# Kernel tuning notes

Hardware: AMD Instinct MI355X
Metric: run time of the kernel (lower is better)

Reference implementation:

```python
import jax, jax.numpy as jnp
import numpy as np
import math

NUM_HEADS = 16
LOGIT_SCALE_MAX = math.log(1.0 / 0.01)  # log(100)
EPS = 1e-12


def _l2norm(x):
    # F.normalize(x, dim=-1): x / max(||x||_2, eps)
    n = jnp.sqrt(jnp.sum(x * x, axis=-1, keepdims=True))
    return x / jnp.maximum(n, EPS)


def setup_inputs() -> dict:
    key = jax.random.key(0)
    ks = jax.random.split(key, 6)
    N, B, C = 1024, 4, 1024
    scale = (C // NUM_HEADS) ** -0.5
    return {
        "query": jax.random.normal(ks[0], (N, B, C), jnp.float32),
        "key": jax.random.normal(ks[1], (N, B, C), jnp.float32),
        "value": jax.random.normal(ks[2], (N, B, C), jnp.float32),
        "in_proj_w": jax.random.normal(ks[3], (3 * C, C), jnp.float32) * scale,
        "in_proj_b": jnp.zeros((3 * C,), jnp.float32),
        "logit_scale": jnp.log(10.0) * jnp.ones((NUM_HEADS, 1, 1), jnp.float32),
        "out_w": jax.random.normal(ks[4], (C, C), jnp.float32) * scale,
        "out_b": jnp.zeros((C,), jnp.float32),
    }


def reference(query, key, value, in_proj_w, in_proj_b, logit_scale, out_w, out_b):
    N, B, C = query.shape
    H = NUM_HEADS
    hd = C // H
    # packed in-projection, split into q/k/v pieces
    w_q, w_k, w_v = jnp.split(in_proj_w, 3, axis=0)
    b_q, b_k, b_v = jnp.split(in_proj_b, 3, axis=0)
    q = query @ w_q.T + b_q          # (N, B, C)
    k = key @ w_k.T + b_k
    v = value @ w_v.T + b_v
    # (N, B, C) -> (B*H, N, hd)
    q = q.reshape(N, B * H, hd).swapaxes(0, 1)
    k = k.reshape(N, B * H, hd).swapaxes(0, 1)
    v = v.reshape(N, B * H, hd).swapaxes(0, 1)
    # cosine-similarity scores with learnable per-head logit scale
    attn = jnp.einsum('bqd,bkd->bqk', _l2norm(q), _l2norm(k))  # (B*H, N, N)
    ls = jnp.exp(jnp.minimum(logit_scale, LOGIT_SCALE_MAX))     # (H,1,1)
    attn = (attn.reshape(B, H, N, N) * ls).reshape(B * H, N, N)
    attn = jax.nn.softmax(attn, axis=-1)
    x = jnp.einsum('bqk,bkd->bqd', attn, v)                     # (B*H, N, hd)
    x = x.swapaxes(0, 1).reshape(N, B, C)
    return x @ out_w.T + out_b
```

## Files before the change

### kernel.cpp

```cpp
#include <hip/hip_runtime.h>


typedef _Float16 f16x8 __attribute__((ext_vector_type(8)));
typedef __fp16   fp16x2 __attribute__((ext_vector_type(2)));
typedef float    f32x4 __attribute__((ext_vector_type(4)));

#define LOG2E 1.4426950408889634f
#define LOGMAX 4.6051702f

#define GLOAD16(g, l) \
    __builtin_amdgcn_global_load_lds((__attribute__((address_space(1))) void*)(g), \
                                     (__attribute__((address_space(3))) void*)(l), 16, 0, 0)

__device__ __forceinline__ unsigned short f2h(float x) {
    union { _Float16 h; unsigned short u; } cv;
    cv.h = (_Float16)x;
    return cv.u;
}

union h2u { fp16x2 h; unsigned int u; };

__global__ __launch_bounds__(256) void cvt_all(
    const float* __restrict__ q, const float* __restrict__ k,
    const float* __restrict__ v, const float* __restrict__ w,
    const float* __restrict__ ow,
    unsigned short* __restrict__ qbf, unsigned short* __restrict__ kbf,
    unsigned short* __restrict__ vbf, unsigned short* __restrict__ wbf,
    unsigned short* __restrict__ owbf)
{
    int b = blockIdx.x;
    const float* src; unsigned short* dst; int idx;
    if      (b < 4096)  { src = q;  dst = qbf;  idx = b; }
    else if (b < 8192)  { src = k;  dst = kbf;  idx = b - 4096; }
    else if (b < 12288) { src = v;  dst = vbf;  idx = b - 8192; }
    else if (b < 15360) { src = w;  dst = wbf;  idx = b - 12288; }
    else                { src = ow; dst = owbf; idx = b - 15360; }
    int i = idx * 256 + threadIdx.x;
    float4 val = ((const float4*)src)[i];
    h2u p01, p23;
    p01.h = __builtin_amdgcn_cvt_pkrtz(val.x, val.y);
    p23.h = __builtin_amdgcn_cvt_pkrtz(val.z, val.w);
    ((uint2*)dst)[i] = (uint2){p01.u, p23.u};
}

__global__ __launch_bounds__(256) void proj_gemm(
    const unsigned short* __restrict__ qbf, const unsigned short* __restrict__ kbf,
    const unsigned short* __restrict__ vbf, const unsigned short* __restrict__ wbf,
    const float* __restrict__ bias, const float* __restrict__ lsc,
    unsigned short* __restrict__ qn, unsigned short* __restrict__ kn,
    unsigned short* __restrict__ vT)
{
    __shared__ __align__(16) unsigned short AsmF[128 * 64];
    __shared__ __align__(16) unsigned short BsmF[128 * 64];
    int tid = threadIdx.x;
    int lane = tid & 63, wave = tid >> 6;
    int lr = lane & 15, lq = lane >> 4;
    int wr = wave >> 1, wc = wave & 1;

    int lin = blockIdx.x;
    int xcd = lin & 7, s = lin >> 3;
    int xt = s & 7, yy = (s >> 3) & 3, z = s >> 5;
    int m0 = (xcd * 4 + yy) * 128, n0 = xt * 128;

    const unsigned short* A = (z == 0) ? qbf : (z == 1) ? kbf : vbf;
    const unsigned short* W = wbf + (size_t)z * 1024 * 1024;

    int rl = lane >> 3;
    int cg = ((lane & 7) ^ rl) << 3;
    const unsigned short* gA = A + (size_t)(m0 + wave * 32 + rl) * 1024 + cg;
    const unsigned short* gB = W + (size_t)(n0 + wave * 32 + rl) * 1024 + cg;
    unsigned short* lA = &AsmF[wave * 32 * 64];
    unsigned short* lB = &BsmF[wave * 32 * 64];

    int swz = lr & 7;
    int c0 = (lq ^ swz) << 3;
    int c1 = ((lq ^ 4) ^ swz) << 3;

    f32x4 acc[4][4];
    for (int i = 0; i < 4; i++) for (int j = 0; j < 4; j++) acc[i][j] = (f32x4){0.f, 0.f, 0.f, 0.f};

    for (int ki = 0; ki < 16; ++ki) {
        for (int j = 0; j < 4; ++j) {
            GLOAD16(gA + ki * 64 + j * 8192, lA + j * 512);
            GLOAD16(gB + ki * 64 + j * 8192, lB + j * 512);
        }
        __syncthreads();
        for (int kc = 0; kc < 2; ++kc) {
            int co = kc ? c1 : c0;
            f16x8 af[4], bfr[4];
            for (int mi = 0; mi < 4; ++mi) af[mi]  = *(const f16x8*)&AsmF[(wr * 64 + mi * 16 + lr) * 64 + co];
            for (int ni = 0; ni < 4; ++ni) bfr[ni] = *(const f16x8*)&BsmF[(wc * 64 + ni * 16 + lr) * 64 + co];
            for (int mi = 0; mi < 4; ++mi)
                for (int ni = 0; ni < 4; ++ni)
                    acc[mi][ni] = __builtin_amdgcn_mfma_f32_16x16x32_f16(af[mi], bfr[ni], acc[mi][ni], 0, 0, 0);
        }
        __syncthreads();
    }

    int h = (n0 >> 6) + wc;
    float bv[4];
    for (int ni = 0; ni < 4; ++ni) bv[ni] = bias[z * 1024 + n0 + wc * 64 + ni * 16 + lr];
    for (int mi = 0; mi < 4; ++mi)
        for (int ni = 0; ni < 4; ++ni)
            for (int r = 0; r < 4; ++r) acc[mi][ni][r] += bv[ni];

    float lsfac = __expf(fminf(lsc[h], LOGMAX)) * LOG2E;

    for (int mi = 0; mi < 4; ++mi)
        for (int r = 0; r < 4; ++r) {
            int row = m0 + wr * 64 + mi * 16 + lq * 4 + r;
            int n = row >> 2, b = row & 3;
            int bh = b * 16 + h;
            if (z < 2) {
                float ss = 0.f;
                for (int ni = 0; ni < 4; ++ni) ss += acc[mi][ni][r] * acc[mi][ni][r];
                for (int off = 1; off < 16; off <<= 1) ss += __shfl_xor(ss, off);
                float scale = 1.0f / fmaxf(sqrtf(ss), 1e-12f);
                if (z == 0) scale *= lsfac;
                unsigned short* dst = (z == 0) ? qn : kn;
                for (int ni = 0; ni < 4; ++ni)
                    dst[(size_t)bh * 65536 + (size_t)n * 64 + ni * 16 + lr] = f2h(acc[mi][ni][r] * scale);
            } else {
                for (int ni = 0; ni < 4; ++ni)
                    vT[(size_t)bh * 65536 + (size_t)(ni * 16 + lr) * 1024 + n] = f2h(acc[mi][ni][r]);
            }
        }
}

__global__ __launch_bounds__(256) void flash_kernel(
    const unsigned short* __restrict__ qn, const unsigned short* __restrict__ kn,
    const unsigned short* __restrict__ vT, const float* __restrict__ lsc,
    unsigned short* __restrict__ xb)
{
    __shared__ __align__(16) unsigned short K_flat[64 * 64];
    __shared__ __align__(16) unsigned short V_flat[64 * 64];
    __shared__ __align__(16) unsigned short P_lds[4][2][16][72];
    int tid = threadIdx.x;
    int lane = tid & 63, wave = tid >> 6;
    int lr = lane & 15, lq = lane >> 4;

    int lin = blockIdx.x;
    int xcd = lin & 7, s = lin >> 3;
    int qt = s & 7, bh = xcd * 8 + (s >> 3);
    int q0 = qt * 128;

    float off = __expf(fminf(lsc[bh & 15], LOGMAX)) * LOG2E - 12.0f;
    f32x4 initv = (f32x4){-off, -off, -off, -off};

    f16x8 onev;
    for (int j = 0; j < 8; ++j) onev[j] = (_Float16)1.0f;

    f16x8 qf[2][2];
    for (int g = 0; g < 2; ++g)
        for (int kc = 0; kc < 2; ++kc)
            qf[g][kc] = *(const f16x8*)(qn + (size_t)bh * 65536 +
                          (size_t)(q0 + g * 64 + wave * 16 + lr) * 64 + kc * 32 + lq * 8);

    int rl = lane >> 3;
    int cg = ((lane & 7) ^ rl) << 3;
    const unsigned short* gK = kn + (size_t)bh * 65536 + (size_t)(wave * 16 + rl) * 64 + cg;
    const unsigned short* gV = vT + (size_t)bh * 65536 + (size_t)(wave * 16 + rl) * 1024 + cg;
    unsigned short* lK = &K_flat[wave * 16 * 64];
    unsigned short* lV = &V_flat[wave * 16 * 64];
    int swz = lr & 7;
    int c0 = (lq ^ swz) << 3;
    int c1 = ((lq ^ 4) ^ swz) << 3;

    f32x4 o[2][4];
    for (int g = 0; g < 2; ++g) for (int i = 0; i < 4; i++) o[g][i] = (f32x4){0.f, 0.f, 0.f, 0.f};
    f32x4 ol[2];
    ol[0] = (f32x4){0.f, 0.f, 0.f, 0.f};
    ol[1] = (f32x4){0.f, 0.f, 0.f, 0.f};

    for (int kt = 0; kt < 16; ++kt) {
        for (int j = 0; j < 2; ++j) {
            GLOAD16(gK + kt * 4096 + j * 512,  lK + j * 512);
            GLOAD16(gV + kt * 64  + j * 8192,  lV + j * 512);
        }
        __syncthreads();

        f32x4 sc[2][4];
        for (int ct = 0; ct < 4; ++ct) {
            for (int kc = 0; kc < 2; ++kc) {
                f16x8 kf = *(const f16x8*)&K_flat[(ct * 16 + lr) * 64 + (kc ? c1 : c0)];
                for (int g = 0; g < 2; ++g)
                    sc[g][ct] = __builtin_amdgcn_mfma_f32_16x16x32_f16(
                        kf, qf[g][kc], kc == 0 ? initv : sc[g][ct], 0, 0, 0);
            }
        }

        for (int g = 0; g < 2; ++g)
            for (int ct = 0; ct < 4; ++ct) {
                float p0 = exp2f(sc[g][ct][0]), p1 = exp2f(sc[g][ct][1]);
                float p2 = exp2f(sc[g][ct][2]), p3 = exp2f(sc[g][ct][3]);
                h2u a01, a23;
                a01.h = __builtin_amdgcn_cvt_pkrtz(p0, p1);
                a23.h = __builtin_amdgcn_cvt_pkrtz(p2, p3);
                *(uint2*)&P_lds[wave][g][lr][ct * 16 + lq * 4] = (uint2){a01.u, a23.u};
            }

        f16x8 pf[2][2];
        for (int g = 0; g < 2; ++g)
            for (int kc = 0; kc < 2; ++kc)
                pf[g][kc] = *(const f16x8*)&P_lds[wave][g][lr][kc * 32 + lq * 8];
        for (int g = 0; g < 2; ++g)
            for (int kc = 0; kc < 2; ++kc)
                ol[g] = __builtin_amdgcn_mfma_f32_16x16x32_f16(onev, pf[g][kc], ol[g], 0, 0, 0);
        for (int nt = 0; nt < 4; ++nt)
            for (int kc = 0; kc < 2; ++kc) {
                f16x8 vf = *(const f16x8*)&V_flat[(nt * 16 + lr) * 64 + (kc ? c1 : c0)];
                for (int g = 0; g < 2; ++g)
                    o[g][nt] = __builtin_amdgcn_mfma_f32_16x16x32_f16(vf, pf[g][kc], o[g][nt], 0, 0, 0);
            }
        __syncthreads();
    }

    int b = bh >> 4, h = bh & 15;
    for (int g = 0; g < 2; ++g) {
        float inv = 1.0f / ol[g][0];
        size_t m = (size_t)(q0 + g * 64 + wave * 16 + lr) * 4 + b;
        h2u w01, w23;
        for (int nt = 0; nt < 4; ++nt) {
            w01.h = __builtin_amdgcn_cvt_pkrtz(o[g][nt][0] * inv, o[g][nt][1] * inv);
            w23.h = __builtin_amdgcn_cvt_pkrtz(o[g][nt][2] * inv, o[g][nt][3] * inv);
            *(uint2*)(xb + m * 1024 + h * 64 + nt * 16 + lq * 4) = (uint2){w01.u, w23.u};
        }
    }
}

__global__ __launch_bounds__(256) void out_gemm(
    const unsigned short* __restrict__ xb, const unsigned short* __restrict__ owbf,
    const float* __restrict__ bias, float* __restrict__ outp)
{
    __shared__ __align__(16) unsigned short AsmF[128 * 64];
    __shared__ __align__(16) unsigned short BsmF[64 * 64];
    int tid = threadIdx.x;
    int lane = tid & 63, wave = tid >> 6;
    int lr = lane & 15, lq = lane >> 4;

    int lin = blockIdx.x;
    int xcd = lin & 7, s = lin >> 3;
    int xt = s & 15, yy = s >> 4;
    int m0 = (xcd * 4 + yy) * 128, n0 = xt * 64;

    int rl = lane >> 3;
    int cg = ((lane & 7) ^ rl) << 3;
    const unsigned short* gA = xb   + (size_t)(m0 + wave * 32 + rl) * 1024 + cg;
    const unsigned short* gB = owbf + (size_t)(n0 + wave * 16 + rl) * 1024 + cg;
    unsigned short* lA = &AsmF[wave * 32 * 64];
    unsigned short* lB = &BsmF[wave * 16 * 64];
    int swz = lr & 7;
    int c0 = (lq ^ swz) << 3;
    int c1 = ((lq ^ 4) ^ swz) << 3;

    f32x4 acc[2][4];
    for (int i = 0; i < 2; i++) for (int j = 0; j < 4; j++) acc[i][j] = (f32x4){0.f, 0.f, 0.f, 0.f};

    for (int ki = 0; ki < 16; ++ki) {
        for (int j = 0; j < 4; ++j)
            GLOAD16(gA + ki * 64 + j * 8192, lA + j * 512);
        for (int j = 0; j < 2; ++j)
            GLOAD16(gB + ki * 64 + j * 8192, lB + j * 512);
        __syncthreads();
        for (int kc = 0; kc < 2; ++kc) {
            int co = kc ? c1 : c0;
            f16x8 af[2], bfr[4];
            for (int mi = 0; mi < 2; ++mi) af[mi]  = *(const f16x8*)&AsmF[(wave * 32 + mi * 16 + lr) * 64 + co];
            for (int ni = 0; ni < 4; ++ni) bfr[ni] = *(const f16x8*)&BsmF[(ni * 16 + lr) * 64 + co];
            for (int mi = 0; mi < 2; ++mi)
                for (int ni = 0; ni < 4; ++ni)
                    acc[mi][ni] = __builtin_amdgcn_mfma_f32_16x16x32_f16(af[mi], bfr[ni], acc[mi][ni], 0, 0, 0);
        }
        __syncthreads();
    }
    for (int mi = 0; mi < 2; ++mi)
        for (int ni = 0; ni < 4; ++ni)
            for (int r = 0; r < 4; ++r) {
                int row = m0 + wave * 32 + mi * 16 + lq * 4 + r;
                int col = n0 + ni * 16 + lr;
                outp[(size_t)row * 1024 + col] = acc[mi][ni][r] + bias[col];
            }
}

extern "C" void kernel_launch(void* const* d_in, const int* in_sizes, int n_in,
                              void* d_out, int out_size, void* d_ws, size_t ws_size,
                              hipStream_t stream) {
    const float* query = (const float*)d_in[0];
    const float* key   = (const float*)d_in[1];
    const float* value = (const float*)d_in[2];
    const float* ipw   = (const float*)d_in[3];
    const float* ipb   = (const float*)d_in[4];
    const float* lsc   = (const float*)d_in[5];
    const float* ow    = (const float*)d_in[6];
    const float* ob    = (const float*)d_in[7];
    float* outp = (float*)d_out;

    char* ws = (char*)d_ws;
    unsigned short* qbf  = (unsigned short*)(ws);
    unsigned short* kbf  = (unsigned short*)(ws + 8388608);
    unsigned short* vbf  = (unsigned short*)(ws + 16777216);
    unsigned short* wbf  = (unsigned short*)(ws + 25165824);
    unsigned short* owbf = (unsigned short*)(ws + 31457280);
    unsigned short* qn   = (unsigned short*)(ws + 33554432);
    unsigned short* kn   = (unsigned short*)(ws + 41943040);
    unsigned short* vT   = (unsigned short*)(ws + 50331648);
    unsigned short* xbuf = (unsigned short*)(ws + 58720256);

    cvt_all<<<16384, 256, 0, stream>>>(query, key, value, ipw, ow,
                                       qbf, kbf, vbf, wbf, owbf);
    proj_gemm<<<768, 256, 0, stream>>>(qbf, kbf, vbf, wbf, ipb, lsc, qn, kn, vT);
    flash_kernel<<<512, 256, 0, stream>>>(qn, kn, vT, lsc, xbuf);
    out_gemm<<<512, 256, 0, stream>>>(xbuf, owbf, ob, outp);
}
```

Before: 210.1 us.

## Double-buffer K/V tiles and keep softmax probabilities in registers for PV MFMA

The flash attention kernel now double-buffers the K and V tiles in LDS. The next tile's global-to-LDS loads are issued before computing on the current one, and one of the two barriers per iteration is removed. The P staging round trip through LDS is dropped: the exp'd scores stay in registers as f16x4 fragments that feed 16x16x16 MFMAs directly, with V fragments read in a matching swizzled layout. This trades a doubled LDS footprint and twice as many narrower MFMA instructions for less LDS traffic and better overlap of loads with compute.

```diff
diff --git a/kernel.cpp b/kernel.cpp
--- a/kernel.cpp
+++ b/kernel.cpp
@@ -2,6 +2,7 @@
 
 
 typedef _Float16 f16x8 __attribute__((ext_vector_type(8)));
+typedef _Float16 f16x4 __attribute__((ext_vector_type(4)));
 typedef __fp16   fp16x2 __attribute__((ext_vector_type(2)));
 typedef float    f32x4 __attribute__((ext_vector_type(4)));
 
@@ -19,6 +20,7 @@
 }
 
 union h2u { fp16x2 h; unsigned int u; };
+union u2h4 { uint2 u; f16x4 h; };
 
 __global__ __launch_bounds__(256) void cvt_all(
     const float* __restrict__ q, const float* __restrict__ k,
@@ -132,9 +134,8 @@
     const unsigned short* __restrict__ vT, const float* __restrict__ lsc,
     unsigned short* __restrict__ xb)
 {
-    __shared__ __align__(16) unsigned short K_flat[64 * 64];
-    __shared__ __align__(16) unsigned short V_flat[64 * 64];
-    __shared__ __align__(16) unsigned short P_lds[4][2][16][72];
+    __shared__ __align__(16) unsigned short K_flat[2][64 * 64];
+    __shared__ __align__(16) unsigned short V_flat[2][64 * 64];
     int tid = threadIdx.x;
     int lane = tid & 63, wave = tid >> 6;
     int lr = lane & 15, lq = lane >> 4;
@@ -147,8 +148,8 @@
     float off = __expf(fminf(lsc[bh & 15], LOGMAX)) * LOG2E - 12.0f;
     f32x4 initv = (f32x4){-off, -off, -off, -off};
 
-    f16x8 onev;
-    for (int j = 0; j < 8; ++j) onev[j] = (_Float16)1.0f;
+    f16x4 onev4;
+    for (int j = 0; j < 4; ++j) onev4[j] = (_Float16)1.0f;
 
     f16x8 qf[2][2];
     for (int g = 0; g < 2; ++g)
@@ -160,8 +161,6 @@
     int cg = ((lane & 7) ^ rl) << 3;
     const unsigned short* gK = kn + (size_t)bh * 65536 + (size_t)(wave * 16 + rl) * 64 + cg;
     const unsigned short* gV = vT + (size_t)bh * 65536 + (size_t)(wave * 16 + rl) * 1024 + cg;
-    unsigned short* lK = &K_flat[wave * 16 * 64];
-    unsigned short* lV = &V_flat[wave * 16 * 64];
     int swz = lr & 7;
     int c0 = (lq ^ swz) << 3;
     int c1 = ((lq ^ 4) ^ swz) << 3;
@@ -172,23 +171,35 @@
     ol[0] = (f32x4){0.f, 0.f, 0.f, 0.f};
     ol[1] = (f32x4){0.f, 0.f, 0.f, 0.f};
 
+    for (int j = 0; j < 2; ++j) {
+        GLOAD16(gK + j * 512,  &K_flat[0][wave * 16 * 64] + j * 512);
+        GLOAD16(gV + j * 8192, &V_flat[0][wave * 16 * 64] + j * 512);
+    }
+
     for (int kt = 0; kt < 16; ++kt) {
-        for (int j = 0; j < 2; ++j) {
-            GLOAD16(gK + kt * 4096 + j * 512,  lK + j * 512);
-            GLOAD16(gV + kt * 64  + j * 8192,  lV + j * 512);
-        }
-        __syncthreads();
+        __syncthreads();
+
+        if (kt < 15) {
+            int nb = (kt + 1) & 1;
+            for (int j = 0; j < 2; ++j) {
+                GLOAD16(gK + (kt + 1) * 4096 + j * 512,  &K_flat[nb][wave * 16 * 64] + j * 512);
+                GLOAD16(gV + (kt + 1) * 64  + j * 8192,  &V_flat[nb][wave * 16 * 64] + j * 512);
+            }
+        }
+        const unsigned short* Kb = K_flat[kt & 1];
+        const unsigned short* Vb = V_flat[kt & 1];
 
         f32x4 sc[2][4];
         for (int ct = 0; ct < 4; ++ct) {
             for (int kc = 0; kc < 2; ++kc) {
-                f16x8 kf = *(const f16x8*)&K_flat[(ct * 16 + lr) * 64 + (kc ? c1 : c0)];
+                f16x8 kf = *(const f16x8*)&Kb[(ct * 16 + lr) * 64 + (kc ? c1 : c0)];
                 for (int g = 0; g < 2; ++g)
                     sc[g][ct] = __builtin_amdgcn_mfma_f32_16x16x32_f16(
                         kf, qf[g][kc], kc == 0 ? initv : sc[g][ct], 0, 0, 0);
             }
         }
 
+        f16x4 ph[2][4];
         for (int g = 0; g < 2; ++g)
             for (int ct = 0; ct < 4; ++ct) {
                 float p0 = exp2f(sc[g][ct][0]), p1 = exp2f(sc[g][ct][1]);
@@ -196,23 +207,21 @@
                 h2u a01, a23;
                 a01.h = __builtin_amdgcn_cvt_pkrtz(p0, p1);
                 a23.h = __builtin_amdgcn_cvt_pkrtz(p2, p3);
-                *(uint2*)&P_lds[wave][g][lr][ct * 16 + lq * 4] = (uint2){a01.u, a23.u};
-            }
-
-        f16x8 pf[2][2];
+                u2h4 pb; pb.u = (uint2){a01.u, a23.u};
+                ph[g][ct] = pb.h;
+            }
+
         for (int g = 0; g < 2; ++g)
-            for (int kc = 0; kc < 2; ++kc)
-                pf[g][kc] = *(const f16x8*)&P_lds[wave][g][lr][kc * 32 + lq * 8];
-        for (int g = 0; g < 2; ++g)
-            for (int kc = 0; kc < 2; ++kc)
-                ol[g] = __builtin_amdgcn_mfma_f32_16x16x32_f16(onev, pf[g][kc], ol[g], 0, 0, 0);
+            for (int ct = 0; ct < 4; ++ct)
+                ol[g] = __builtin_amdgcn_mfma_f32_16x16x16f16(onev4, ph[g][ct], ol[g], 0, 0, 0);
+
         for (int nt = 0; nt < 4; ++nt)
-            for (int kc = 0; kc < 2; ++kc) {
-                f16x8 vf = *(const f16x8*)&V_flat[(nt * 16 + lr) * 64 + (kc ? c1 : c0)];
+            for (int ct = 0; ct < 4; ++ct) {
+                int vc = (((2 * ct + (lq >> 1)) ^ swz) << 3) + ((lq & 1) << 2);
+                f16x4 vf = *(const f16x4*)&Vb[(nt * 16 + lr) * 64 + vc];
                 for (int g = 0; g < 2; ++g)
-                    o[g][nt] = __builtin_amdgcn_mfma_f32_16x16x32_f16(vf, pf[g][kc], o[g][nt], 0, 0, 0);
-            }
-        __syncthreads();
+                    o[g][nt] = __builtin_amdgcn_mfma_f32_16x16x16f16(vf, ph[g][ct], o[g][nt], 0, 0, 0);
+            }
     }
 
     int b = bh >> 4, h = bh & 15;
```

Measured after the change: 209.7 us. Within noise of the previous version (-0.2%).
